# Kernel optimization log

Hardware: AMD Instinct MI355X
Metric: run time of the kernel (lower is better)

## Reference

```python
import jax, jax.numpy as jnp
import numpy as np

SEQ_LEN = 2048
EMB = 512
BATCH = 8


def _xavier_uniform(key, shape):
    fan_in, fan_out = shape[0], shape[1]
    bound = float(np.sqrt(6.0 / (fan_in + fan_out)))
    return jax.random.uniform(key, shape, dtype=jnp.float32, minval=-bound, maxval=bound)


def setup_inputs() -> dict:
    key = jax.random.key(0)
    kx, k1, k2 = jax.random.split(key, 3)
    x = jax.random.normal(kx, (BATCH, EMB, SEQ_LEN), dtype=jnp.float32)
    weight1 = _xavier_uniform(k1, (EMB, EMB))
    weight2 = _xavier_uniform(k2, (EMB, EMB))
    return {"x": x, "weight1": weight1, "weight2": weight2}


def reference(x, weight1, weight2):
    # x: [b, e, s]
    s = x.shape[-1]
    # projections: O(b*s*e^2)
    fitnesses1 = jnp.einsum('bes,ef->bfs', x, weight1)   # [b, e, s]
    fitnesses2 = jnp.einsum('bfs,ef->bes', x, weight2)   # [b, e, s]
    # s x t interaction matrix: O(b*s^2*e)
    weight = jnp.einsum('bes,bet->bst', fitnesses1, fitnesses2)  # [b, s, t]
    # zero strictly-upper triangle (t > s), as in torch.triu(..., diagonal=1)
    mask = jnp.triu(jnp.ones((s, s), dtype=bool), k=1)
    weight = jnp.where(mask, jnp.zeros((), dtype=weight.dtype), weight)
    fitnesses = jnp.einsum('bst,bet->bes', weight, x)    # [b, e, s]
    avg_fitness = jnp.einsum('bes,bes->be', x, fitnesses)[..., None]  # [b, e, 1]
    net_fitnesses = fitnesses - avg_fitness
    x_next = x + x * net_fitnesses
    return jax.nn.relu(x_next)
```

## Files before the change

kernel.cpp:

```cpp
#include <hip/hip_runtime.h>
#include <hip/hip_bf16.h>
#include <stdint.h>


#define SEQ 2048
#define EMB 512
#define NBATCH 8

typedef unsigned short u16;
typedef __bf16 bf16x8 __attribute__((ext_vector_type(8)));
typedef float f32x4 __attribute__((ext_vector_type(4)));
typedef u16 u16x8 __attribute__((ext_vector_type(8)));

#define AS1 __attribute__((address_space(1)))
#define AS3 __attribute__((address_space(3)))

#define SBAR do { __builtin_amdgcn_sched_barrier(0); __builtin_amdgcn_s_barrier(); \
                  __builtin_amdgcn_sched_barrier(0); } while (0)
#define LGKM0 do { asm volatile("s_waitcnt lgkmcnt(0)" ::: "memory"); \
                   __builtin_amdgcn_sched_barrier(0); } while (0)

__device__ __forceinline__ u16 f2bf(float f) {
  uint32_t u = __builtin_bit_cast(uint32_t, f);
  uint32_t r = u + 0x7FFFu + ((u >> 16) & 1u);
  return (u16)(r >> 16);
}
__device__ __forceinline__ float bf2f(u16 u) {
  return __builtin_bit_cast(float, (uint32_t)u << 16);
}

__device__ __forceinline__ void gld_lds16(const void* g, void* l) {
  __builtin_amdgcn_global_load_lds((AS1 uint32_t*)g, (AS3 uint32_t*)l, 16, 0, 0);
}

__global__ __launch_bounds__(256) void prep_x_kernel(const float* __restrict__ x,
    u16* __restrict__ xb, u16* __restrict__ xbT) {
  __shared__ float tile[64][65];
  const int b = blockIdx.z;
  const int s0 = blockIdx.x * 64, e0 = blockIdx.y * 64;
  const float* xin = x + (size_t)b * EMB * SEQ;
  const int tid = threadIdx.x;
  #pragma unroll
  for (int it = 0; it < 4; ++it) {
    int idx = it * 256 + tid;
    int r = idx >> 4, c4 = idx & 15;
    float4 v = *(const float4*)(xin + (size_t)(e0 + r) * SEQ + s0 + c4 * 4);
    tile[r][c4 * 4 + 0] = v.x; tile[r][c4 * 4 + 1] = v.y;
    tile[r][c4 * 4 + 2] = v.z; tile[r][c4 * 4 + 3] = v.w;
  }
  __syncthreads();
  u16* ob = xb + (size_t)b * EMB * SEQ;
  #pragma unroll
  for (int it = 0; it < 2; ++it) {
    int idx = it * 256 + tid; int r = idx >> 3, c8 = idx & 7;
    u16x8 o;
    #pragma unroll
    for (int q = 0; q < 8; ++q) o[q] = f2bf(tile[r][c8 * 8 + q]);
    *(u16x8*)(ob + (size_t)(e0 + r) * SEQ + s0 + c8 * 8) = o;
  }
  u16* obT = xbT + (size_t)b * SEQ * EMB;
  #pragma unroll
  for (int it = 0; it < 2; ++it) {
    int idx = it * 256 + tid; int r = idx >> 3, c8 = idx & 7;
    u16x8 o;
    #pragma unroll
    for (int q = 0; q < 8; ++q) o[q] = f2bf(tile[c8 * 8 + q][r]);
    *(u16x8*)(obT + (size_t)(s0 + r) * EMB + e0 + c8 * 8) = o;
  }
}

__global__ __launch_bounds__(256) void cast_bf16_kernel(const float* __restrict__ in,
                                                        u16* __restrict__ out, int n4) {
  int i = blockIdx.x * 256 + threadIdx.x;
  if (i >= n4) return;
  float4 v = reinterpret_cast<const float4*>(in)[i];
  ushort4 r;
  r.x = f2bf(v.x); r.y = f2bf(v.y); r.z = f2bf(v.z); r.w = f2bf(v.w);
  reinterpret_cast<ushort4*>(out)[i] = r;
}

__global__ __launch_bounds__(256) void transpose_cast_kernel(const float* __restrict__ in,
    u16* __restrict__ out, int R, int C) {
  __shared__ float tile[32][33];
  const int c0 = blockIdx.x * 32, r0 = blockIdx.y * 32;
  const int tx = threadIdx.x, ty = threadIdx.y;
  #pragma unroll
  for (int i = 0; i < 32; i += 8)
    tile[ty + i][tx] = in[(size_t)(r0 + ty + i) * C + c0 + tx];
  __syncthreads();
  #pragma unroll
  for (int i = 0; i < 32; i += 8)
    out[(size_t)(c0 + ty + i) * R + r0 + tx] = f2bf(tile[tx][ty + i]);
}

template<int MODE>
__global__ __launch_bounds__(512, 2) void gemm8_kernel(
    const u16* __restrict__ Ag, const u16* __restrict__ Bg, void* __restrict__ Cg,
    float* __restrict__ P1out, float* __restrict__ P2out,
    int ldA, int ldB, int ldC, long sA, long sB, long sC, int Kfull) {
  const int tid  = threadIdx.x;
  const int lane = tid & 63;
  const int wave = tid >> 6;
  const int wr = wave >> 2;
  const int wc = wave & 3;
  const int bz = blockIdx.z;

  int bm, bn, k0, kend, dest = 0;
  if (MODE == 0) {
    bm = blockIdx.x; bn = blockIdx.y; k0 = 0; kend = Kfull;
  } else if (MODE == 1) {
    int xx = blockIdx.x;
    int c = xx & 7, ii = xx >> 3;
    int tile = (c < 4) ? (c * 5 + ii) : (20 + (c - 4) * 4 + ii);
    int L = tile, i = 0;
    while (L >= i + 1) { L -= i + 1; ++i; }
    bm = i; bn = L; k0 = 0; kend = Kfull;
  } else {
    static const int tj[15]  = {0,1,2,3,4,5,6,7, 3,4,5,6,7, 6,7};
    static const int tk0[15] = {0,0,0,0,0,0,0,0, 768,768,768,768,768, 1536,1536};
    static const int tk1[15] = {256,512,768,768,768,768,768,768, 1024,1280,1536,1536,1536, 1792,2048};
    static const int tds[15] = {0,0,0,0,0,0,0,0, 1,1,1,1,1, 2,2};
    const int L = blockIdx.y;
    bm = blockIdx.x; bn = tj[L]; k0 = tk0[L]; kend = tk1[L]; dest = tds[L];
  }
  const int nk = (kend - k0) >> 6;

  const u16* Ab = Ag + (size_t)bz * sA + (size_t)(bm * 256) * ldA;
  const u16* Bb = Bg + (size_t)bz * sB + (size_t)(bn * 256) * ldB;

  __shared__ __align__(16) u16 LA[2][256 * 64];
  __shared__ __align__(16) u16 LB[2][256 * 64];

  auto stage_half = [&](const u16* gbase, int ldG, int rowOff, int kcol, u16* lds) {
    #pragma unroll
    for (int p = 0; p < 2; ++p) {
      int c = p * 512 + tid;
      int row = c >> 3, cc = c & 7;
      int cs = cc ^ (row & 7);
      gld_lds16(gbase + (size_t)(rowOff + row) * ldG + kcol + cs * 8,
                lds + (size_t)(p * 512 + wave * 64) * 8);
    }
  };

  auto ldfrag = [&](const u16* base, int rloc, int c2) -> bf16x8 {
    int cs = c2 ^ (rloc & 7);
    return *reinterpret_cast<const bf16x8*>(base + (size_t)(rloc * 8 + cs) * 8);
  };

  f32x4 acc[8][4];
  #pragma unroll
  for (int i = 0; i < 8; ++i)
    #pragma unroll
    for (int j = 0; j < 4; ++j) acc[i][j] = (f32x4){0.f, 0.f, 0.f, 0.f};

  stage_half(Ab, ldA, 0,   k0, LA[0]);
  stage_half(Ab, ldA, 128, k0, LA[0] + 8192);
  stage_half(Bb, ldB, 0,   k0, LB[0]);
  stage_half(Bb, ldB, 128, k0, LB[0] + 8192);
  if (nk > 1) {
    stage_half(Bb, ldB, 0,   k0 + 64, LB[1]);
    stage_half(Bb, ldB, 128, k0 + 64, LB[1] + 8192);
  }
  if (nk > 1) { asm volatile("s_waitcnt vmcnt(4)" ::: "memory"); }
  else        { asm volatile("s_waitcnt vmcnt(0)" ::: "memory"); }
  SBAR;

  const int ar = lane & 15;
  const int asel = lane >> 4;

  bf16x8 af[4][2], bf0[2][2], bf1[2][2];

  for (int t = 0; t < nk; ++t) {
    const int sel = t & 1;
    const u16* a_ = LA[sel];
    const u16* b_ = LB[sel];

    #pragma unroll
    for (int m = 0; m < 4; ++m)
      #pragma unroll
      for (int kk = 0; kk < 2; ++kk)
        af[m][kk] = ldfrag(a_, wr * 128 + m * 16 + ar, kk * 4 + asel);
    #pragma unroll
    for (int n = 0; n < 2; ++n)
      #pragma unroll
      for (int kk = 0; kk < 2; ++kk)
        bf0[n][kk] = ldfrag(b_, wc * 64 + n * 16 + ar, kk * 4 + asel);
    if (t + 1 < nk) stage_half(Ab, ldA, 0, k0 + (t + 1) * 64, LA[sel ^ 1]);
    SBAR; LGKM0;
    __builtin_amdgcn_s_setprio(1);
    #pragma unroll
    for (int m = 0; m < 4; ++m)
      #pragma unroll
      for (int n = 0; n < 2; ++n)
        #pragma unroll
        for (int kk = 0; kk < 2; ++kk)
          acc[m][n] = __builtin_amdgcn_mfma_f32_16x16x32_bf16(af[m][kk], bf0[n][kk], acc[m][n], 0, 0, 0);
    __builtin_amdgcn_s_setprio(0);
    SBAR;

    #pragma unroll
    for (int n = 0; n < 2; ++n)
      #pragma unroll
      for (int kk = 0; kk < 2; ++kk)
        bf1[n][kk] = ldfrag(b_, wc * 64 + (n + 2) * 16 + ar, kk * 4 + asel);
    if (t + 1 < nk) stage_half(Ab, ldA, 128, k0 + (t + 1) * 64, LA[sel ^ 1] + 8192);
    SBAR; LGKM0;
    __builtin_amdgcn_s_setprio(1);
    #pragma unroll
    for (int m = 0; m < 4; ++m)
      #pragma unroll
      for (int n = 0; n < 2; ++n)
        #pragma unroll
        for (int kk = 0; kk < 2; ++kk)
          acc[m][n + 2] = __builtin_amdgcn_mfma_f32_16x16x32_bf16(af[m][kk], bf1[n][kk], acc[m][n + 2], 0, 0, 0);
    __builtin_amdgcn_s_setprio(0);
    SBAR;

    #pragma unroll
    for (int m = 0; m < 4; ++m)
      #pragma unroll
      for (int kk = 0; kk < 2; ++kk)
        af[m][kk] = ldfrag(a_, wr * 128 + 64 + m * 16 + ar, kk * 4 + asel);
    if (t + 2 < nk) stage_half(Bb, ldB, 0, k0 + (t + 2) * 64, LB[sel]);
    SBAR; LGKM0;
    __builtin_amdgcn_s_setprio(1);
    #pragma unroll
    for (int m = 0; m < 4; ++m)
      #pragma unroll
      for (int n = 0; n < 2; ++n)
        #pragma unroll
        for (int kk = 0; kk < 2; ++kk)
          acc[m + 4][n + 2] = __builtin_amdgcn_mfma_f32_16x16x32_bf16(af[m][kk], bf1[n][kk], acc[m + 4][n + 2], 0, 0, 0);
    __builtin_amdgcn_s_setprio(0);
    SBAR;

    if (t + 2 < nk) stage_half(Bb, ldB, 128, k0 + (t + 2) * 64, LB[sel] + 8192);
    SBAR;
    __builtin_amdgcn_s_setprio(1);
    #pragma unroll
    for (int m = 0; m < 4; ++m)
      #pragma unroll
      for (int n = 0; n < 2; ++n)
        #pragma unroll
        for (int kk = 0; kk < 2; ++kk)
          acc[m + 4][n] = __builtin_amdgcn_mfma_f32_16x16x32_bf16(af[m][kk], bf0[n][kk], acc[m + 4][n], 0, 0, 0);
    __builtin_amdgcn_s_setprio(0);
    if (t + 1 < nk) {
      if (t + 2 < nk) { asm volatile("s_waitcnt vmcnt(4)" ::: "memory"); }
      else            { asm volatile("s_waitcnt vmcnt(0)" ::: "memory"); }
    }
    SBAR;
  }

  const int r0 = (lane >> 4) * 4;
  const int cn = lane & 15;
  #pragma unroll
  for (int m = 0; m < 8; ++m) {
    #pragma unroll
    for (int n = 0; n < 4; ++n) {
      const int gcol = bn * 256 + wc * 64 + n * 16 + cn;
      #pragma unroll
      for (int r = 0; r < 4; ++r) {
        const int grow = bm * 256 + wr * 128 + m * 16 + r0 + r;
        float v = acc[m][n][r];
        if (MODE == 2) {
          float* base; int ldc, coff;
          if (dest == 0)      { base = (float*)Cg + (size_t)bz * sC; ldc = SEQ;  coff = 0; }
          else if (dest == 1) { base = P1out + (size_t)bz * (512 * 1280); ldc = 1280; coff = 768; }
          else                { base = P2out + (size_t)bz * (512 * 512);  ldc = 512;  coff = 1536; }
          base[(size_t)grow * ldc + (gcol - coff)] = v;
        } else {
          if (MODE == 1 && bm == bn && gcol > grow) v = 0.f;
          ((u16*)Cg)[(size_t)bz * sC + (size_t)grow * ldC + gcol] = f2bf(v);
        }
      }
    }
  }
}

__global__ __launch_bounds__(256) void finalize_kernel(const u16* __restrict__ xb,
    const float* __restrict__ fit, const float* __restrict__ fitP,
    const float* __restrict__ fitP2, float* __restrict__ out) {
  const size_t row = blockIdx.x;
  const u16* xr = xb + row * SEQ;
  const float* fr = fit + row * SEQ;
  const float* p1 = fitP + row * 1280;
  const float* p2 = fitP2 + row * 512;
  float* orow = out + row * SEQ;
  const int tid = threadIdx.x;

  float xv[2][4]; float4 fv[2];
  float part = 0.f;
  #pragma unroll
  for (int i = 0; i < 2; ++i) {
    const int s0 = i * 1024 + tid * 4;
    ushort4 xu = *reinterpret_cast<const ushort4*>(xr + s0);
    xv[i][0] = bf2f(xu.x); xv[i][1] = bf2f(xu.y); xv[i][2] = bf2f(xu.z); xv[i][3] = bf2f(xu.w);
    fv[i] = reinterpret_cast<const float4*>(fr)[i * 256 + tid];
    if (s0 >= 768) {
      float4 a = *reinterpret_cast<const float4*>(p1 + (s0 - 768));
      fv[i].x += a.x; fv[i].y += a.y; fv[i].z += a.z; fv[i].w += a.w;
    }
    if (s0 >= 1536) {
      float4 a = *reinterpret_cast<const float4*>(p2 + (s0 - 1536));
      fv[i].x += a.x; fv[i].y += a.y; fv[i].z += a.z; fv[i].w += a.w;
    }
    part += xv[i][0] * fv[i].x + xv[i][1] * fv[i].y + xv[i][2] * fv[i].z + xv[i][3] * fv[i].w;
  }
  #pragma unroll
  for (int off = 1; off < 64; off <<= 1) part += __shfl_xor(part, off);
  __shared__ float wsum[4];
  const int wave = tid >> 6, lane = tid & 63;
  if (lane == 0) wsum[wave] = part;
  __syncthreads();
  const float avg = wsum[0] + wsum[1] + wsum[2] + wsum[3];

  #pragma unroll
  for (int i = 0; i < 2; ++i) {
    float4 o;
    o.x = xv[i][0] * (1.f + fv[i].x - avg); o.x = o.x > 0.f ? o.x : 0.f;
    o.y = xv[i][1] * (1.f + fv[i].y - avg); o.y = o.y > 0.f ? o.y : 0.f;
    o.z = xv[i][2] * (1.f + fv[i].z - avg); o.z = o.z > 0.f ? o.z : 0.f;
    o.w = xv[i][3] * (1.f + fv[i].w - avg); o.w = o.w > 0.f ? o.w : 0.f;
    reinterpret_cast<float4*>(orow)[i * 256 + tid] = o;
  }
}

extern "C" void kernel_launch(void* const* d_in, const int* in_sizes, int n_in,
                              void* d_out, int out_size, void* d_ws, size_t ws_size,
                              hipStream_t stream) {
  const float* x  = (const float*)d_in[0];
  const float* W1 = (const float*)d_in[1];
  const float* W2 = (const float*)d_in[2];
  float* out = (float*)d_out;

  char* ws = (char*)d_ws;
  const size_t nX = (size_t)NBATCH * EMB * SEQ;

  size_t off = 0;
  u16* xb   = (u16*)(ws + off); off += nX * 2;
  const size_t offFit = off;
  u16* xbT  = (u16*)(ws + off); off += nX * 2;
  u16* Wcat = (u16*)(ws + off); off += (size_t)1024 * 512 * 2;
  u16* Fcat = (u16*)(ws + off); off += (size_t)NBATCH * SEQ * 1024 * 2;
  u16* Wm   = (u16*)(ws + off); off += (size_t)NBATCH * SEQ * SEQ * 2;
  float* fitP  = (float*)(ws + off); off += (size_t)NBATCH * 512 * 1280 * 4;
  float* fitP2 = (float*)(ws + off); off += (size_t)NBATCH * 512 * 512 * 4;
  float* fit = (float*)(ws + offFit);

  prep_x_kernel<<<dim3(SEQ / 64, EMB / 64, NBATCH), 256, 0, stream>>>(x, xb, xbT);
  transpose_cast_kernel<<<dim3(EMB / 32, EMB / 32), dim3(32, 8), 0, stream>>>(W1, Wcat, EMB, EMB);
  cast_bf16_kernel<<<EMB * EMB / 4 / 256, 256, 0, stream>>>(W2, Wcat + (size_t)512 * 512, EMB * EMB / 4);

  gemm8_kernel<0><<<dim3(8, 4, NBATCH), 512, 0, stream>>>(
      xbT, Wcat, Fcat, nullptr, nullptr, EMB, EMB, 1024, (long)SEQ * EMB, 0, (long)SEQ * 1024, EMB);

  gemm8_kernel<1><<<dim3(36, 1, NBATCH), 512, 0, stream>>>(
      Fcat, Fcat + 512, Wm, nullptr, nullptr, 1024, 1024, SEQ,
      (long)SEQ * 1024, (long)SEQ * 1024, (long)SEQ * SEQ, EMB);

  gemm8_kernel<2><<<dim3(2, 15, NBATCH), 512, 0, stream>>>(
      xb, Wm, fit, fitP, fitP2, SEQ, SEQ, SEQ,
      (long)EMB * SEQ, (long)SEQ * SEQ, (long)EMB * SEQ, SEQ);

  finalize_kernel<<<NBATCH * EMB, 256, 0, stream>>>(xb, fit, fitP, fitP2, out);
}
```

Before: 135.7 us.

## Reassociate causal interaction via blockwise prefix sums of x·F2ᵀ Gram blocks

Replaces the explicit s×s masked interaction matrix and its lower-triangular multiply with a reassociated form. The code computes per-chunk Gram matrices G_j = x_j F2_jᵀ (e×e), prefix-sums them across sequence chunks, and multiplies the prefix by F1 for the off-diagonal blocks. Only the 256×256 diagonal blocks are formed explicitly and masked. This removes the O(s²e) work and the large bf16 Wm buffer in favour of O(s·e²) work plus a small prefix kernel. The cost is extra launches and bf16 rounding of the accumulated prefix sums, which may reduce accuracy.

Result: no change. 133.7 us (-1.5%).

```diff
diff --git a/kernel.cpp b/kernel.cpp
--- a/kernel.cpp
+++ b/kernel.cpp
@@ -28,7 +28,6 @@
 __device__ __forceinline__ float bf2f(u16 u) {
   return __builtin_bit_cast(float, (uint32_t)u << 16);
 }
-
 __device__ __forceinline__ void gld_lds16(const void* g, void* l) {
   __builtin_amdgcn_global_load_lds((AS1 uint32_t*)g, (AS3 uint32_t*)l, 16, 0, 0);
 }
@@ -93,43 +92,18 @@
     out[(size_t)(c0 + ty + i) * R + r0 + tx] = f2bf(tile[tx][ty + i]);
 }
 
-template<int MODE>
-__global__ __launch_bounds__(512, 2) void gemm8_kernel(
-    const u16* __restrict__ Ag, const u16* __restrict__ Bg, void* __restrict__ Cg,
-    float* __restrict__ P1out, float* __restrict__ P2out,
-    int ldA, int ldB, int ldC, long sA, long sB, long sC, int Kfull) {
+struct Smem {
+  __align__(16) u16 LA[2][256 * 64];
+  __align__(16) u16 LB[2][256 * 64];
+};
+
+__device__ __forceinline__ void gemm_pipe(const u16* __restrict__ Ab, int ldA,
+    const u16* __restrict__ Bb, int ldB, int nk, Smem& sm, f32x4 (&acc)[8][4]) {
   const int tid  = threadIdx.x;
   const int lane = tid & 63;
   const int wave = tid >> 6;
   const int wr = wave >> 2;
   const int wc = wave & 3;
-  const int bz = blockIdx.z;
-
-  int bm, bn, k0, kend, dest = 0;
-  if (MODE == 0) {
-    bm = blockIdx.x; bn = blockIdx.y; k0 = 0; kend = Kfull;
-  } else if (MODE == 1) {
-    int xx = blockIdx.x;
-    int c = xx & 7, ii = xx >> 3;
-    int tile = (c < 4) ? (c * 5 + ii) : (20 + (c - 4) * 4 + ii);
-    int L = tile, i = 0;
-    while (L >= i + 1) { L -= i + 1; ++i; }
-    bm = i; bn = L; k0 = 0; kend = Kfull;
-  } else {
-    static const int tj[15]  = {0,1,2,3,4,5,6,7, 3,4,5,6,7, 6,7};
-    static const int tk0[15] = {0,0,0,0,0,0,0,0, 768,768,768,768,768, 1536,1536};
-    static const int tk1[15] = {256,512,768,768,768,768,768,768, 1024,1280,1536,1536,1536, 1792,2048};
-    static const int tds[15] = {0,0,0,0,0,0,0,0, 1,1,1,1,1, 2,2};
-    const int L = blockIdx.y;
-    bm = blockIdx.x; bn = tj[L]; k0 = tk0[L]; kend = tk1[L]; dest = tds[L];
-  }
-  const int nk = (kend - k0) >> 6;
-
-  const u16* Ab = Ag + (size_t)bz * sA + (size_t)(bm * 256) * ldA;
-  const u16* Bb = Bg + (size_t)bz * sB + (size_t)(bn * 256) * ldB;
-
-  __shared__ __align__(16) u16 LA[2][256 * 64];
-  __shared__ __align__(16) u16 LB[2][256 * 64];
 
   auto stage_half = [&](const u16* gbase, int ldG, int rowOff, int kcol, u16* lds) {
     #pragma unroll
@@ -141,25 +115,18 @@
                 lds + (size_t)(p * 512 + wave * 64) * 8);
     }
   };
-
   auto ldfrag = [&](const u16* base, int rloc, int c2) -> bf16x8 {
     int cs = c2 ^ (rloc & 7);
     return *reinterpret_cast<const bf16x8*>(base + (size_t)(rloc * 8 + cs) * 8);
   };
 
-  f32x4 acc[8][4];
-  #pragma unroll
-  for (int i = 0; i < 8; ++i)
-    #pragma unroll
-    for (int j = 0; j < 4; ++j) acc[i][j] = (f32x4){0.f, 0.f, 0.f, 0.f};
-
-  stage_half(Ab, ldA, 0,   k0, LA[0]);
-  stage_half(Ab, ldA, 128, k0, LA[0] + 8192);
-  stage_half(Bb, ldB, 0,   k0, LB[0]);
-  stage_half(Bb, ldB, 128, k0, LB[0] + 8192);
+  stage_half(Ab, ldA, 0,   0, sm.LA[0]);
+  stage_half(Ab, ldA, 128, 0, sm.LA[0] + 8192);
+  stage_half(Bb, ldB, 0,   0, sm.LB[0]);
+  stage_half(Bb, ldB, 128, 0, sm.LB[0] + 8192);
   if (nk > 1) {
-    stage_half(Bb, ldB, 0,   k0 + 64, LB[1]);
-    stage_half(Bb, ldB, 128, k0 + 64, LB[1] + 8192);
+    stage_half(Bb, ldB, 0,   64, sm.LB[1]);
+    stage_half(Bb, ldB, 128, 64, sm.LB[1] + 8192);
   }
   if (nk > 1) { asm volatile("s_waitcnt vmcnt(4)" ::: "memory"); }
   else        { asm volatile("s_waitcnt vmcnt(0)" ::: "memory"); }
@@ -167,13 +134,12 @@
 
   const int ar = lane & 15;
   const int asel = lane >> 4;
-
   bf16x8 af[4][2], bf0[2][2], bf1[2][2];
 
   for (int t = 0; t < nk; ++t) {
     const int sel = t & 1;
-    const u16* a_ = LA[sel];
-    const u16* b_ = LB[sel];
+    const u16* a_ = sm.LA[sel];
+    const u16* b_ = sm.LB[sel];
 
     #pragma unroll
     for (int m = 0; m < 4; ++m)
@@ -185,7 +151,7 @@
       #pragma unroll
       for (int kk = 0; kk < 2; ++kk)
         bf0[n][kk] = ldfrag(b_, wc * 64 + n * 16 + ar, kk * 4 + asel);
-    if (t + 1 < nk) stage_half(Ab, ldA, 0, k0 + (t + 1) * 64, LA[sel ^ 1]);
+    if (t + 1 < nk) stage_half(Ab, ldA, 0, (t + 1) * 64, sm.LA[sel ^ 1]);
     SBAR; LGKM0;
     __builtin_amdgcn_s_setprio(1);
     #pragma unroll
@@ -203,7 +169,7 @@
       #pragma unroll
       for (int kk = 0; kk < 2; ++kk)
         bf1[n][kk] = ldfrag(b_, wc * 64 + (n + 2) * 16 + ar, kk * 4 + asel);
-    if (t + 1 < nk) stage_half(Ab, ldA, 128, k0 + (t + 1) * 64, LA[sel ^ 1] + 8192);
+    if (t + 1 < nk) stage_half(Ab, ldA, 128, (t + 1) * 64, sm.LA[sel ^ 1] + 8192);
     SBAR; LGKM0;
     __builtin_amdgcn_s_setprio(1);
     #pragma unroll
@@ -221,7 +187,7 @@
       #pragma unroll
       for (int kk = 0; kk < 2; ++kk)
         af[m][kk] = ldfrag(a_, wr * 128 + 64 + m * 16 + ar, kk * 4 + asel);
-    if (t + 2 < nk) stage_half(Bb, ldB, 0, k0 + (t + 2) * 64, LB[sel]);
+    if (t + 2 < nk) stage_half(Bb, ldB, 0, (t + 2) * 64, sm.LB[sel]);
     SBAR; LGKM0;
     __builtin_amdgcn_s_setprio(1);
     #pragma unroll
@@ -234,7 +200,7 @@
     __builtin_amdgcn_s_setprio(0);
     SBAR;
 
-    if (t + 2 < nk) stage_half(Bb, ldB, 128, k0 + (t + 2) * 64, LB[sel] + 8192);
+    if (t + 2 < nk) stage_half(Bb, ldB, 128, (t + 2) * 64, sm.LB[sel] + 8192);
     SBAR;
     __builtin_amdgcn_s_setprio(1);
     #pragma unroll
@@ -251,41 +217,141 @@
     }
     SBAR;
   }
+}
+
+template<int MODE>
+__global__ __launch_bounds__(512, 2) void k_gemm(
+    const u16* __restrict__ X1, const u16* __restrict__ X2,
+    const u16* __restrict__ X3, const u16* __restrict__ X4,
+    u16* __restrict__ O16, u16* __restrict__ O16b, float* __restrict__ O32) {
+  __shared__ Smem sm;
+  const int tid  = threadIdx.x;
+  const int lane = tid & 63;
+  const int wave = tid >> 6;
+  const int wr = wave >> 2;
+  const int wc = wave & 3;
+  const int bz = blockIdx.z;
+
+  f32x4 acc[8][4];
+  #pragma unroll
+  for (int i = 0; i < 8; ++i)
+    #pragma unroll
+    for (int j = 0; j < 4; ++j) acc[i][j] = (f32x4){0.f, 0.f, 0.f, 0.f};
 
   const int r0 = (lane >> 4) * 4;
   const int cn = lane & 15;
-  #pragma unroll
-  for (int m = 0; m < 8; ++m) {
-    #pragma unroll
-    for (int n = 0; n < 4; ++n) {
-      const int gcol = bn * 256 + wc * 64 + n * 16 + cn;
-      #pragma unroll
-      for (int r = 0; r < 4; ++r) {
-        const int grow = bm * 256 + wr * 128 + m * 16 + r0 + r;
-        float v = acc[m][n][r];
-        if (MODE == 2) {
-          float* base; int ldc, coff;
-          if (dest == 0)      { base = (float*)Cg + (size_t)bz * sC; ldc = SEQ;  coff = 0; }
-          else if (dest == 1) { base = P1out + (size_t)bz * (512 * 1280); ldc = 1280; coff = 768; }
-          else                { base = P2out + (size_t)bz * (512 * 512);  ldc = 512;  coff = 1536; }
-          base[(size_t)grow * ldc + (gcol - coff)] = v;
-        } else {
-          if (MODE == 1 && bm == bn && gcol > grow) v = 0.f;
-          ((u16*)Cg)[(size_t)bz * sC + (size_t)grow * ldC + gcol] = f2bf(v);
+
+  if (MODE == 0) {
+    const int bm = blockIdx.x, bn = blockIdx.y;
+    const u16* A = X1 + (size_t)bz * SEQ * EMB + (size_t)(bm * 256) * 512;
+    const u16* B = X2 + (size_t)(bn * 256) * 512;
+    gemm_pipe(A, 512, B, 512, 8, sm, acc);
+    u16* C = O16 + (size_t)bz * SEQ * 1024;
+    #pragma unroll
+    for (int m = 0; m < 8; ++m)
+      #pragma unroll
+      for (int n = 0; n < 4; ++n)
+        #pragma unroll
+        for (int r = 0; r < 4; ++r) {
+          int lr = wr * 128 + m * 16 + r0 + r, lc = wc * 64 + n * 16 + cn;
+          C[(size_t)(bm * 256 + lr) * 1024 + bn * 256 + lc] = f2bf(acc[m][n][r]);
         }
-      }
+  } else if (MODE == 1) {
+    const int xx = blockIdx.x;
+    if (xx < 16) {
+      const int m2 = xx >> 3, n2 = xx & 7;
+      const u16* A = X1 + (size_t)(m2 * 256) * 512;
+      const u16* B = X2 + (size_t)bz * SEQ * EMB + (size_t)(n2 * 256) * 512;
+      gemm_pipe(A, 512, B, 512, 8, sm, acc);
+      u16* C = O16 + (size_t)bz * EMB * SEQ;
+      #pragma unroll
+      for (int m = 0; m < 8; ++m)
+        #pragma unroll
+        for (int n = 0; n < 4; ++n)
+          #pragma unroll
+          for (int r = 0; r < 4; ++r) {
+            int lr = wr * 128 + m * 16 + r0 + r, lc = wc * 64 + n * 16 + cn;
+            C[(size_t)(m2 * 256 + lr) * SEQ + n2 * 256 + lc] = f2bf(acc[m][n][r]);
+          }
+    } else {
+      const int i = xx - 16;
+      const u16* Fb = X3 + (size_t)bz * SEQ * 1024;
+      const u16* A = Fb + (size_t)(i * 256) * 1024;
+      const u16* B = Fb + 512 + (size_t)(i * 256) * 1024;
+      gemm_pipe(A, 1024, B, 1024, 8, sm, acc);
+      u16* C = O16b + (size_t)(bz * 8 + i) * 256 * 256;
+      #pragma unroll
+      for (int m = 0; m < 8; ++m)
+        #pragma unroll
+        for (int n = 0; n < 4; ++n)
+          #pragma unroll
+          for (int r = 0; r < 4; ++r) {
+            int lr = wr * 128 + m * 16 + r0 + r, lc = wc * 64 + n * 16 + cn;
+            float v = (lc > lr) ? 0.f : acc[m][n][r];
+            C[(size_t)lr * 256 + lc] = f2bf(v);
+          }
     }
+  } else if (MODE == 2) {
+    const int m = blockIdx.x >> 1, n = blockIdx.x & 1;
+    const int b = bz >> 3, j = bz & 7;
+    const u16* A = X1 + (size_t)b * EMB * SEQ + (size_t)(m * 256) * SEQ + j * 256;
+    const u16* B = X2 + (size_t)b * EMB * SEQ + (size_t)(n * 256) * SEQ + j * 256;
+    gemm_pipe(A, SEQ, B, SEQ, 4, sm, acc);
+    u16* C = O16 + (size_t)(b * 8 + j) * EMB * EMB;
+    #pragma unroll
+    for (int mm = 0; mm < 8; ++mm)
+      #pragma unroll
+      for (int nn = 0; nn < 4; ++nn)
+        #pragma unroll
+        for (int r = 0; r < 4; ++r) {
+          int lr = wr * 128 + mm * 16 + r0 + r, lc = wc * 64 + nn * 16 + cn;
+          C[(size_t)(m * 256 + lr) * EMB + n * 256 + lc] = f2bf(acc[mm][nn][r]);
+        }
+  } else {
+    const int m = blockIdx.x & 1, i = blockIdx.x >> 1;
+    if (i > 0) {
+      const u16* A = X1 + (size_t)(bz * 7 + i - 1) * EMB * EMB + (size_t)(m * 256) * 512;
+      const u16* B = X2 + (size_t)bz * SEQ * 1024 + (size_t)(i * 256) * 1024;
+      gemm_pipe(A, 512, B, 1024, 8, sm, acc);
+    }
+    {
+      const u16* A = X3 + (size_t)bz * EMB * SEQ + (size_t)(m * 256) * SEQ + i * 256;
+      const u16* B = X4 + (size_t)(bz * 8 + i) * 256 * 256;
+      gemm_pipe(A, SEQ, B, 256, 4, sm, acc);
+    }
+    float* C = O32 + (size_t)bz * EMB * SEQ;
+    #pragma unroll
+    for (int mm = 0; mm < 8; ++mm)
+      #pragma unroll
+      for (int nn = 0; nn < 4; ++nn)
+        #pragma unroll
+        for (int r = 0; r < 4; ++r) {
+          int lr = wr * 128 + mm * 16 + r0 + r, lc = wc * 64 + nn * 16 + cn;
+          C[(size_t)(m * 256 + lr) * SEQ + i * 256 + lc] = acc[mm][nn][r];
+        }
+  }
+}
+
+__global__ __launch_bounds__(256) void k_prefix(const u16* __restrict__ Gc,
+                                                u16* __restrict__ Gp) {
+  const int b = blockIdx.z;
+  const size_t base = ((size_t)blockIdx.x * 256 + threadIdx.x) * 8;
+  float run[8] = {0.f, 0.f, 0.f, 0.f, 0.f, 0.f, 0.f, 0.f};
+  #pragma unroll
+  for (int j = 0; j < 7; ++j) {
+    u16x8 v = *(const u16x8*)(Gc + (size_t)(b * 8 + j) * EMB * EMB + base);
+    u16x8 o;
+    #pragma unroll
+    for (int q = 0; q < 8; ++q) { run[q] += bf2f(v[q]); o[q] = f2bf(run[q]); }
+    *(u16x8*)(Gp + (size_t)(b * 7 + j) * EMB * EMB + base) = o;
   }
 }
 
 __global__ __launch_bounds__(256) void finalize_kernel(const u16* __restrict__ xb,
-    const float* __restrict__ fit, const float* __restrict__ fitP,
-    const float* __restrict__ fitP2, float* __restrict__ out) {
+    const float* __restrict__ fit, float* __restrict__ out) {
   const size_t row = blockIdx.x;
   const u16* xr = xb + row * SEQ;
   const float* fr = fit + row * SEQ;
-  const float* p1 = fitP + row * 1280;
-  const float* p2 = fitP2 + row * 512;
   float* orow = out + row * SEQ;
   const int tid = threadIdx.x;
 
@@ -297,14 +363,6 @@
     ushort4 xu = *reinterpret_cast<const ushort4*>(xr + s0);
     xv[i][0] = bf2f(xu.x); xv[i][1] = bf2f(xu.y); xv[i][2] = bf2f(xu.z); xv[i][3] = bf2f(xu.w);
     fv[i] = reinterpret_cast<const float4*>(fr)[i * 256 + tid];
-    if (s0 >= 768) {
-      float4 a = *reinterpret_cast<const float4*>(p1 + (s0 - 768));
-      fv[i].x += a.x; fv[i].y += a.y; fv[i].z += a.z; fv[i].w += a.w;
-    }
-    if (s0 >= 1536) {
-      float4 a = *reinterpret_cast<const float4*>(p2 + (s0 - 1536));
-      fv[i].x += a.x; fv[i].y += a.y; fv[i].z += a.z; fv[i].w += a.w;
-    }
     part += xv[i][0] * fv[i].x + xv[i][1] * fv[i].y + xv[i][2] * fv[i].z + xv[i][3] * fv[i].w;
   }
   #pragma unroll
@@ -339,29 +397,33 @@
 
   size_t off = 0;
   u16* xb   = (u16*)(ws + off); off += nX * 2;
-  const size_t offFit = off;
+  u16* Fcat = (u16*)(ws + off); off += (size_t)NBATCH * SEQ * 1024 * 2;
+  const size_t offOverlay = off;
   u16* xbT  = (u16*)(ws + off); off += nX * 2;
   u16* Wcat = (u16*)(ws + off); off += (size_t)1024 * 512 * 2;
-  u16* Fcat = (u16*)(ws + off); off += (size_t)NBATCH * SEQ * 1024 * 2;
-  u16* Wm   = (u16*)(ws + off); off += (size_t)NBATCH * SEQ * SEQ * 2;
-  float* fitP  = (float*)(ws + off); off += (size_t)NBATCH * 512 * 1280 * 4;
-  float* fitP2 = (float*)(ws + off); off += (size_t)NBATCH * 512 * 512 * 4;
-  float* fit = (float*)(ws + offFit);
+  u16* F2n  = (u16*)(ws + off); off += nX * 2;
+  u16* Sd   = (u16*)(ws + off); off += (size_t)NBATCH * 8 * 256 * 256 * 2;
+  u16* Gc   = (u16*)(ws + off); off += (size_t)NBATCH * 8 * EMB * EMB * 2;
+  u16* Gp   = (u16*)(ws + off); off += (size_t)NBATCH * 7 * EMB * EMB * 2;
+  float* fit = (float*)(ws + offOverlay);
 
   prep_x_kernel<<<dim3(SEQ / 64, EMB / 64, NBATCH), 256, 0, stream>>>(x, xb, xbT);
   transpose_cast_kernel<<<dim3(EMB / 32, EMB / 32), dim3(32, 8), 0, stream>>>(W1, Wcat, EMB, EMB);
   cast_bf16_kernel<<<EMB * EMB / 4 / 256, 256, 0, stream>>>(W2, Wcat + (size_t)512 * 512, EMB * EMB / 4);
 
-  gemm8_kernel<0><<<dim3(8, 4, NBATCH), 512, 0, stream>>>(
-      xbT, Wcat, Fcat, nullptr, nullptr, EMB, EMB, 1024, (long)SEQ * EMB, 0, (long)SEQ * 1024, EMB);
-
-  gemm8_kernel<1><<<dim3(36, 1, NBATCH), 512, 0, stream>>>(
-      Fcat, Fcat + 512, Wm, nullptr, nullptr, 1024, 1024, SEQ,
-      (long)SEQ * 1024, (long)SEQ * 1024, (long)SEQ * SEQ, EMB);
-
-  gemm8_kernel<2><<<dim3(2, 15, NBATCH), 512, 0, stream>>>(
-      xb, Wm, fit, fitP, fitP2, SEQ, SEQ, SEQ,
-      (long)EMB * SEQ, (long)SEQ * SEQ, (long)EMB * SEQ, SEQ);
-
-  finalize_kernel<<<NBATCH * EMB, 256, 0, stream>>>(xb, fit, fitP, fitP2, out);
-}
+  k_gemm<0><<<dim3(8, 4, NBATCH), 512, 0, stream>>>(
+      xbT, Wcat, nullptr, nullptr, Fcat, nullptr, nullptr);
+
+  k_gemm<1><<<dim3(24, 1, NBATCH), 512, 0, stream>>>(
+      Wcat + (size_t)512 * 512, xbT, Fcat, nullptr, F2n, Sd, nullptr);
+
+  k_gemm<2><<<dim3(4, 1, 64), 512, 0, stream>>>(
+      xb, F2n, nullptr, nullptr, Gc, nullptr, nullptr);
+
+  k_prefix<<<dim3(128, 1, NBATCH), 256, 0, stream>>>(Gc, Gp);
+
+  k_gemm<3><<<dim3(16, 1, NBATCH), 512, 0, stream>>>(
+      Gp, Fcat, xb, Sd, nullptr, nullptr, fit);
+
+  finalize_kernel<<<NBATCH * EMB, 256, 0, stream>>>(xb, fit, out);
+}
```
